# Kernel tuning notes

Hardware: AMD Instinct MI355X
Metric: run time of the kernel (lower is better)

Reference implementation:

```python
import jax, jax.numpy as jnp
import numpy as np

N, E, F, D = 50000, 800000, 128, 32
CUTOFF = 5.0


def swish(x):
    return x * jax.nn.sigmoid(x)


def setup_inputs() -> dict:
    key = jax.random.key(0)
    ks = jax.random.split(key, 15)
    sF = 1.0 / np.sqrt(F)
    inp = {
        "x": jax.random.normal(ks[0], (N, F), jnp.float32),
        # distances in [0, 6) so some edges lie beyond the 5.0 cutoff
        "rij": jax.random.uniform(ks[1], (E,), jnp.float32) * 6.0,
        "vij": jax.random.normal(ks[2], (E, 3), jnp.float32),
        "src": jax.random.randint(ks[3], (E,), 0, N),
        "dst": jax.random.randint(ks[4], (E,), 0, N),
        # transform: Dense(F,F,swish) -> Dense(F,D,swish)
        "W1": jax.random.normal(ks[5], (F, F), jnp.float32) * sF,
        "b1": jnp.zeros((F,), jnp.float32),
        "W2": jax.random.normal(ks[6], (F, D), jnp.float32) * sF,
        "b2": jnp.zeros((D,), jnp.float32),
        # transform2 (cross_product branch)
        "W1b": jax.random.normal(ks[7], (F, F), jnp.float32) * sF,
        "b1b": jnp.zeros((F,), jnp.float32),
        "W2b": jax.random.normal(ks[8], (F, D), jnp.float32) * sF,
        "b2b": jnp.zeros((D,), jnp.float32),
        # mix: Dense(3, 1), no activation
        "w_mix": jax.random.normal(ks[9], (3,), jnp.float32) * (1.0 / np.sqrt(3.0)),
        "b_mix": jnp.zeros((1,), jnp.float32),
    }
    return inp


def reference(x, rij, vij, src, dst, W1, b1, W2, b2, W1b, b1b, W2b, b2b, w_mix, b_mix):
    # node transforms: q, q2 in [N, D]
    q = swish(swish(x @ W1 + b1) @ W2 + b2)
    q2 = swish(swish(x @ W1b + b1b) @ W2b + b2b)

    # cosine cutoff on per-edge distance [E]
    c = 0.5 * (jnp.cos(jnp.pi * rij / CUTOFF) + 1.0)
    c = c * (rij < CUTOFF).astype(c.dtype)

    # e_mul_u: edge vij [E,1,3] * source-node q [E,D,1] -> [E,D,3], then cutoff scale
    mu_ij = vij[:, None, :] * q[src][:, :, None] * c[:, None, None]
    mu = jax.ops.segment_sum(mu_ij, dst, num_segments=N)  # [N,D,3]

    mu_ij2 = vij[:, None, :] * q2[src][:, :, None] * c[:, None, None]
    mu2 = jax.ops.segment_sum(mu_ij2, dst, num_segments=N)  # [N,D,3]

    mu3 = jnp.cross(mu, mu2, axis=-1)  # [N,D,3]
    stacked = jnp.stack([mu, mu2, mu3], axis=-1)  # [N,D,3,3]
    out = stacked @ w_mix + b_mix[0]  # mix Dense(3,1), squeezed -> [N,D,3]
    return out
```

## Files before the change

kernel.cpp:

```cpp
#include <hip/hip_runtime.h>
#include <hip/hip_bf16.h>

#define N_NODES 50000
#define E_EDGES 800000
#define F_DIM 128
#define D_DIM 32
#define CUTOFF 5.0f
#define PI_F 3.14159265358979f
#define SCAN_BLOCKS ((N_NODES + 255) / 256)

#define MLP_ROWBLOCKS 782
#define MLP_BLOCKS (MLP_ROWBLOCKS * 2)
#define HIST_BLOCKS ((E_EDGES + 511) / 512)
#define XPAD 132

__device__ __forceinline__ float swishf(float x) { return x / (1.0f + expf(-x)); }

__global__ __launch_bounds__(512, 4)
void mlp_hist(const float* __restrict__ x,
              const float* __restrict__ W1a, const float* __restrict__ b1a,
              const float* __restrict__ W2a, const float* __restrict__ b2a,
              const float* __restrict__ W1b, const float* __restrict__ b1b,
              const float* __restrict__ W2b, const float* __restrict__ b2b,
              float* __restrict__ qq,
              const float* __restrict__ rij, const int* __restrict__ dst,
              int* __restrict__ deg) {
  if (blockIdx.x >= MLP_BLOCKS) {
    const int e = (blockIdx.x - MLP_BLOCKS) * 512 + threadIdx.x;
    if (e < E_EDGES && rij[e] < CUTOFF) atomicAdd(&deg[dst[e]], 1);
    return;
  }

  __shared__ float sX[64 * XPAD];

  const int bid = blockIdx.x;
  const int br  = (bid >= MLP_ROWBLOCKS) ? 1 : 0;
  const int rb  = (bid - br * MLP_ROWBLOCKS) * 64;

  const float* __restrict__ W1 = br ? W1b : W1a;
  const float* __restrict__ b1 = br ? b1b : b1a;
  const float* __restrict__ W2 = br ? W2b : W2a;
  const float* __restrict__ b2 = br ? b2b : b2a;

  const int t = threadIdx.x;
  const int l = t & 63;
  const int w = t >> 6;

  {
    const int row = t >> 3;
    const int kq  = t & 7;
    const int rowG = min(rb + row, N_NODES - 1);
    const float* xp = x + (size_t)rowG * F_DIM;
#pragma unroll
    for (int p = 0; p < 4; ++p) {
      const int k0 = kq * 4 + p * 32;
      *(float4*)&sX[row * XPAD + k0] = *(const float4*)&xp[k0];
    }
  }
  __syncthreads();

  const int cb = l & 31;
  const int g  = (w << 1) + (l >> 5);
  const int r0 = g * 4;

  float acc[4][4];
#pragma unroll
  for (int j = 0; j < 4; ++j) {
    const float bj = b1[cb + 32 * j];
#pragma unroll
    for (int r = 0; r < 4; ++r) acc[r][j] = bj;
  }
  {
    const float* xrow = sX + r0 * XPAD;
#pragma unroll 2
    for (int k4 = 0; k4 < 32; ++k4) {
      float4 xv[4];
#pragma unroll
      for (int r = 0; r < 4; ++r)
        xv[r] = *(const float4*)&xrow[r * XPAD + k4 * 4];
#pragma unroll
      for (int kk = 0; kk < 4; ++kk) {
        const int k = k4 * 4 + kk;
        float wv[4];
#pragma unroll
        for (int j = 0; j < 4; ++j)
          wv[j] = W1[(size_t)k * F_DIM + cb + 32 * j];
#pragma unroll
        for (int r = 0; r < 4; ++r) {
          const float xs = (kk == 0) ? xv[r].x : (kk == 1) ? xv[r].y
                         : (kk == 2) ? xv[r].z : xv[r].w;
#pragma unroll
          for (int j = 0; j < 4; ++j)
            acc[r][j] = fmaf(xs, wv[j], acc[r][j]);
        }
      }
    }
  }

  __syncthreads();
#pragma unroll
  for (int r = 0; r < 4; ++r)
#pragma unroll
    for (int j = 0; j < 4; ++j)
      sX[(r0 + r) * XPAD + cb + 32 * j] = swishf(acc[r][j]);
  __syncthreads();

  float acc2[4];
  {
    const float b2c = b2[cb];
#pragma unroll
    for (int r = 0; r < 4; ++r) acc2[r] = b2c;
  }
  {
    const float* hrow = sX + r0 * XPAD;
#pragma unroll 2
    for (int k4 = 0; k4 < 32; ++k4) {
      float4 hv[4];
#pragma unroll
      for (int r = 0; r < 4; ++r)
        hv[r] = *(const float4*)&hrow[r * XPAD + k4 * 4];
#pragma unroll
      for (int kk = 0; kk < 4; ++kk) {
        const float wv = W2[(size_t)(k4 * 4 + kk) * D_DIM + cb];
#pragma unroll
        for (int r = 0; r < 4; ++r) {
          const float hs = (kk == 0) ? hv[r].x : (kk == 1) ? hv[r].y
                         : (kk == 2) ? hv[r].z : hv[r].w;
          acc2[r] = fmaf(hs, wv, acc2[r]);
        }
      }
    }
  }
#pragma unroll
  for (int r = 0; r < 4; ++r) {
    const int row = rb + r0 + r;
    if (row < N_NODES) qq[(size_t)row * 64 + 2 * cb + br] = swishf(acc2[r]);
  }
}

__global__ __launch_bounds__(256)
void scan_blocksum(const int* __restrict__ deg, int* __restrict__ part) {
  __shared__ int red[256];
  const int t = threadIdx.x;
  const int i = blockIdx.x * 256 + t;
  red[t] = (i < N_NODES) ? deg[i] : 0;
  __syncthreads();
#pragma unroll
  for (int off = 128; off > 0; off >>= 1) {
    if (t < off) red[t] += red[t + off];
    __syncthreads();
  }
  if (t == 0) part[blockIdx.x] = red[0];
}

__global__ __launch_bounds__(256)
void scan_partials(int* __restrict__ part, int* __restrict__ row_start) {
  __shared__ int s[256];
  const int t = threadIdx.x;
  const int v = (t < SCAN_BLOCKS) ? part[t] : 0;
  s[t] = v;
  __syncthreads();
  for (int off = 1; off < 256; off <<= 1) {
    const int u = (t >= off) ? s[t - off] : 0;
    __syncthreads();
    s[t] += u;
    __syncthreads();
  }
  if (t < SCAN_BLOCKS) part[t] = s[t] - v;
  if (t == 255) row_start[N_NODES] = s[255];
}

__global__ __launch_bounds__(256)
void scan_write(const int* __restrict__ deg, const int* __restrict__ part,
                int* __restrict__ row_start, int* __restrict__ cursor) {
  __shared__ int s[256];
  const int t = threadIdx.x;
  const int i = blockIdx.x * 256 + t;
  const int v = (i < N_NODES) ? deg[i] : 0;
  s[t] = v;
  __syncthreads();
  for (int off = 1; off < 256; off <<= 1) {
    const int u = (t >= off) ? s[t - off] : 0;
    __syncthreads();
    s[t] += u;
    __syncthreads();
  }
  const int excl = s[t] - v + part[blockIdx.x];
  if (i < N_NODES) { row_start[i] = excl; cursor[i] = excl; }
}

__global__ __launch_bounds__(256)
void edge_reorder(const float* __restrict__ rij, const float* __restrict__ vij,
                  const int* __restrict__ src, const int* __restrict__ dst,
                  int* __restrict__ cursor, float4* __restrict__ recs) {
  const int e = blockIdx.x * 256 + threadIdx.x;
  if (e >= E_EDGES) return;
  const float r = rij[e];
  if (r >= CUTOFF) return;
  const float c = 0.5f * (cosf(r * (PI_F / CUTOFF)) + 1.0f);
  const int pos = atomicAdd(&cursor[dst[e]], 1);
  recs[pos] = make_float4(c * vij[3 * e + 0], c * vij[3 * e + 1],
                          c * vij[3 * e + 2], __int_as_float(src[e]));
}

__global__ __launch_bounds__(256)
void gather_out(const int* __restrict__ row_start, const float4* __restrict__ recs,
                const float2* __restrict__ qq,
                const float* __restrict__ w_mix, const float* __restrict__ b_mix,
                float* __restrict__ out) {
  const int tid = blockIdx.x * 256 + threadIdx.x;
  const int n = tid >> 5;
  const int d = tid & 31;
  if (n >= N_NODES) return;

  const int s0 = row_start[n];
  const int s1 = row_start[n + 1];

  float ax = 0.f, ay = 0.f, az = 0.f, bx = 0.f, by = 0.f, bz = 0.f;
  for (int i = s0; i < s1; i += 4) {
    const int i1 = min(i + 1, s1 - 1);
    const int i2 = min(i + 2, s1 - 1);
    const int i3 = min(i + 3, s1 - 1);
    float4 rc0 = recs[i];
    float4 rc1 = recs[i1];
    float4 rc2 = recs[i2];
    float4 rc3 = recs[i3];
    float2 p0 = qq[__float_as_int(rc0.w) * 32 + d];
    float2 p1 = qq[__float_as_int(rc1.w) * 32 + d];
    float2 p2 = qq[__float_as_int(rc2.w) * 32 + d];
    float2 p3 = qq[__float_as_int(rc3.w) * 32 + d];
    const float m1 = (i + 1 < s1) ? 1.f : 0.f;
    const float m2 = (i + 2 < s1) ? 1.f : 0.f;
    const float m3 = (i + 3 < s1) ? 1.f : 0.f;
    p1.x *= m1; p1.y *= m1;
    p2.x *= m2; p2.y *= m2;
    p3.x *= m3; p3.y *= m3;

    ax += rc0.x * p0.x + rc1.x * p1.x + rc2.x * p2.x + rc3.x * p3.x;
    ay += rc0.y * p0.x + rc1.y * p1.x + rc2.y * p2.x + rc3.y * p3.x;
    az += rc0.z * p0.x + rc1.z * p1.x + rc2.z * p2.x + rc3.z * p3.x;
    bx += rc0.x * p0.y + rc1.x * p1.y + rc2.x * p2.y + rc3.x * p3.y;
    by += rc0.y * p0.y + rc1.y * p1.y + rc2.y * p2.y + rc3.y * p3.y;
    bz += rc0.z * p0.y + rc1.z * p1.y + rc2.z * p2.y + rc3.z * p3.y;
  }

  const float cx = ay * bz - az * by;
  const float cy = az * bx - ax * bz;
  const float cz = ax * by - ay * bx;

  const float w0 = w_mix[0], w1 = w_mix[1], w2 = w_mix[2];
  const float bm = b_mix[0];

  const size_t base = (size_t)tid * 3;
  out[base + 0] = ax * w0 + bx * w1 + cx * w2 + bm;
  out[base + 1] = ay * w0 + by * w1 + cy * w2 + bm;
  out[base + 2] = az * w0 + bz * w1 + cz * w2 + bm;
}

extern "C" void kernel_launch(void* const* d_in, const int* in_sizes, int n_in,
                              void* d_out, int out_size, void* d_ws, size_t ws_size,
                              hipStream_t stream) {
  const float* x     = (const float*)d_in[0];
  const float* rij   = (const float*)d_in[1];
  const float* vij   = (const float*)d_in[2];
  const int*   src   = (const int*)  d_in[3];
  const int*   dst   = (const int*)  d_in[4];
  const float* W1    = (const float*)d_in[5];
  const float* b1    = (const float*)d_in[6];
  const float* W2    = (const float*)d_in[7];
  const float* b2    = (const float*)d_in[8];
  const float* W1b   = (const float*)d_in[9];
  const float* b1b   = (const float*)d_in[10];
  const float* W2b   = (const float*)d_in[11];
  const float* b2b   = (const float*)d_in[12];
  const float* w_mix = (const float*)d_in[13];
  const float* b_mix = (const float*)d_in[14];
  float* out = (float*)d_out;

  float4* recs   = (float4*)d_ws;
  float* qq      = (float*)(recs + E_EDGES);
  int* deg       = (int*)(qq + (size_t)N_NODES * 64);
  int* cursor    = deg + N_NODES;
  int* row_start = cursor + N_NODES;
  int* part      = row_start + N_NODES + 1;

  hipMemsetAsync(deg, 0, sizeof(int) * N_NODES, stream);

  mlp_hist<<<MLP_BLOCKS + HIST_BLOCKS, 512, 0, stream>>>(
      x, W1, b1, W2, b2, W1b, b1b, W2b, b2b, qq, rij, dst, deg);

  scan_blocksum<<<SCAN_BLOCKS, 256, 0, stream>>>(deg, part);
  scan_partials<<<1, 256, 0, stream>>>(part, row_start);
  scan_write<<<SCAN_BLOCKS, 256, 0, stream>>>(deg, part, row_start, cursor);

  const int eb = (E_EDGES + 255) / 256;
  edge_reorder<<<eb, 256, 0, stream>>>(rij, vij, src, dst, cursor, recs);

  gather_out<<<(N_NODES * D_DIM) / 256, 256, 0, stream>>>(
      row_start, recs, (const float2*)qq, w_mix, b_mix, out);
}
```

Measured before the change: 280.0 us.

## Compute both MLP branches per block with larger per-thread register tiles

```diff
diff --git a/kernel.cpp b/kernel.cpp
--- a/kernel.cpp
+++ b/kernel.cpp
@@ -9,14 +9,13 @@
 #define PI_F 3.14159265358979f
 #define SCAN_BLOCKS ((N_NODES + 255) / 256)
 
-#define MLP_ROWBLOCKS 782
-#define MLP_BLOCKS (MLP_ROWBLOCKS * 2)
-#define HIST_BLOCKS ((E_EDGES + 511) / 512)
+#define MLP_BLOCKS ((N_NODES + 63) / 64)
+#define HIST_BLOCKS ((E_EDGES + 255) / 256)
 #define XPAD 132
 
 __device__ __forceinline__ float swishf(float x) { return x / (1.0f + expf(-x)); }
 
-__global__ __launch_bounds__(512, 4)
+__global__ __launch_bounds__(256, 4)
 void mlp_hist(const float* __restrict__ x,
               const float* __restrict__ W1a, const float* __restrict__ b1a,
               const float* __restrict__ W2a, const float* __restrict__ b2a,
@@ -26,115 +25,145 @@
               const float* __restrict__ rij, const int* __restrict__ dst,
               int* __restrict__ deg) {
   if (blockIdx.x >= MLP_BLOCKS) {
-    const int e = (blockIdx.x - MLP_BLOCKS) * 512 + threadIdx.x;
+    const int e = (blockIdx.x - MLP_BLOCKS) * 256 + threadIdx.x;
     if (e < E_EDGES && rij[e] < CUTOFF) atomicAdd(&deg[dst[e]], 1);
     return;
   }
 
   __shared__ float sX[64 * XPAD];
 
-  const int bid = blockIdx.x;
-  const int br  = (bid >= MLP_ROWBLOCKS) ? 1 : 0;
-  const int rb  = (bid - br * MLP_ROWBLOCKS) * 64;
-
-  const float* __restrict__ W1 = br ? W1b : W1a;
-  const float* __restrict__ b1 = br ? b1b : b1a;
-  const float* __restrict__ W2 = br ? W2b : W2a;
-  const float* __restrict__ b2 = br ? b2b : b2a;
-
-  const int t = threadIdx.x;
-  const int l = t & 63;
-  const int w = t >> 6;
-
-  {
-    const int row = t >> 3;
-    const int kq  = t & 7;
+  const int rb = blockIdx.x * 64;
+  const int t  = threadIdx.x;
+  const int c16 = t & 15;
+  const int r0  = (t >> 4) * 4;
+
+  float qo[2][4][2];
+
+  auto stage_x = [&]() {
+    const int row = t >> 2;
+    const int kq  = t & 3;
     const int rowG = min(rb + row, N_NODES - 1);
     const float* xp = x + (size_t)rowG * F_DIM;
 #pragma unroll
-    for (int p = 0; p < 4; ++p) {
-      const int k0 = kq * 4 + p * 32;
+    for (int p = 0; p < 8; ++p) {
+      const int k0 = kq * 4 + p * 16;
       *(float4*)&sX[row * XPAD + k0] = *(const float4*)&xp[k0];
     }
-  }
-  __syncthreads();
-
-  const int cb = l & 31;
-  const int g  = (w << 1) + (l >> 5);
-  const int r0 = g * 4;
-
-  float acc[4][4];
-#pragma unroll
-  for (int j = 0; j < 4; ++j) {
-    const float bj = b1[cb + 32 * j];
-#pragma unroll
-    for (int r = 0; r < 4; ++r) acc[r][j] = bj;
-  }
-  {
-    const float* xrow = sX + r0 * XPAD;
+  };
+
+#pragma unroll
+  for (int br = 0; br < 2; ++br) {
+    const float* __restrict__ W1 = br ? W1b : W1a;
+    const float* __restrict__ b1 = br ? b1b : b1a;
+    const float* __restrict__ W2 = br ? W2b : W2a;
+    const float* __restrict__ b2 = br ? b2b : b2a;
+
+    if (br) __syncthreads();
+    stage_x();
+    __syncthreads();
+
+    float acc[4][8];
+    {
+      const float4 bv0 = *(const float4*)&b1[8 * c16];
+      const float4 bv1 = *(const float4*)&b1[8 * c16 + 4];
+#pragma unroll
+      for (int r = 0; r < 4; ++r) {
+        acc[r][0] = bv0.x; acc[r][1] = bv0.y; acc[r][2] = bv0.z; acc[r][3] = bv0.w;
+        acc[r][4] = bv1.x; acc[r][5] = bv1.y; acc[r][6] = bv1.z; acc[r][7] = bv1.w;
+      }
+    }
+    {
+      const float* xrow  = sX + r0 * XPAD;
+      const float* wbase = W1 + 8 * c16;
 #pragma unroll 2
-    for (int k4 = 0; k4 < 32; ++k4) {
-      float4 xv[4];
-#pragma unroll
-      for (int r = 0; r < 4; ++r)
-        xv[r] = *(const float4*)&xrow[r * XPAD + k4 * 4];
-#pragma unroll
-      for (int kk = 0; kk < 4; ++kk) {
-        const int k = k4 * 4 + kk;
-        float wv[4];
-#pragma unroll
-        for (int j = 0; j < 4; ++j)
-          wv[j] = W1[(size_t)k * F_DIM + cb + 32 * j];
-#pragma unroll
-        for (int r = 0; r < 4; ++r) {
-          const float xs = (kk == 0) ? xv[r].x : (kk == 1) ? xv[r].y
-                         : (kk == 2) ? xv[r].z : xv[r].w;
-#pragma unroll
-          for (int j = 0; j < 4; ++j)
-            acc[r][j] = fmaf(xs, wv[j], acc[r][j]);
+      for (int k4 = 0; k4 < 32; ++k4) {
+        float4 w0[4], w1[4];
+#pragma unroll
+        for (int kk = 0; kk < 4; ++kk) {
+          const float* wp = wbase + (size_t)(k4 * 4 + kk) * F_DIM;
+          w0[kk] = *(const float4*)wp;
+          w1[kk] = *(const float4*)(wp + 4);
+        }
+        float4 xv[4];
+#pragma unroll
+        for (int r = 0; r < 4; ++r)
+          xv[r] = *(const float4*)&xrow[r * XPAD + k4 * 4];
+#pragma unroll
+        for (int kk = 0; kk < 4; ++kk) {
+#pragma unroll
+          for (int r = 0; r < 4; ++r) {
+            const float xs = (kk == 0) ? xv[r].x : (kk == 1) ? xv[r].y
+                           : (kk == 2) ? xv[r].z : xv[r].w;
+            acc[r][0] = fmaf(xs, w0[kk].x, acc[r][0]);
+            acc[r][1] = fmaf(xs, w0[kk].y, acc[r][1]);
+            acc[r][2] = fmaf(xs, w0[kk].z, acc[r][2]);
+            acc[r][3] = fmaf(xs, w0[kk].w, acc[r][3]);
+            acc[r][4] = fmaf(xs, w1[kk].x, acc[r][4]);
+            acc[r][5] = fmaf(xs, w1[kk].y, acc[r][5]);
+            acc[r][6] = fmaf(xs, w1[kk].z, acc[r][6]);
+            acc[r][7] = fmaf(xs, w1[kk].w, acc[r][7]);
+          }
         }
       }
     }
-  }
-
-  __syncthreads();
-#pragma unroll
-  for (int r = 0; r < 4; ++r)
-#pragma unroll
-    for (int j = 0; j < 4; ++j)
-      sX[(r0 + r) * XPAD + cb + 32 * j] = swishf(acc[r][j]);
-  __syncthreads();
-
-  float acc2[4];
-  {
-    const float b2c = b2[cb];
-#pragma unroll
-    for (int r = 0; r < 4; ++r) acc2[r] = b2c;
-  }
-  {
-    const float* hrow = sX + r0 * XPAD;
+
+    __syncthreads();
+#pragma unroll
+    for (int r = 0; r < 4; ++r) {
+      *(float4*)&sX[(r0 + r) * XPAD + 8 * c16] =
+          make_float4(swishf(acc[r][0]), swishf(acc[r][1]),
+                      swishf(acc[r][2]), swishf(acc[r][3]));
+      *(float4*)&sX[(r0 + r) * XPAD + 8 * c16 + 4] =
+          make_float4(swishf(acc[r][4]), swishf(acc[r][5]),
+                      swishf(acc[r][6]), swishf(acc[r][7]));
+    }
+    __syncthreads();
+
+    float a2[4][2];
+    {
+      const float2 b2v = *(const float2*)&b2[2 * c16];
+#pragma unroll
+      for (int r = 0; r < 4; ++r) { a2[r][0] = b2v.x; a2[r][1] = b2v.y; }
+    }
+    {
+      const float* hrow = sX + r0 * XPAD;
 #pragma unroll 2
-    for (int k4 = 0; k4 < 32; ++k4) {
-      float4 hv[4];
-#pragma unroll
-      for (int r = 0; r < 4; ++r)
-        hv[r] = *(const float4*)&hrow[r * XPAD + k4 * 4];
-#pragma unroll
-      for (int kk = 0; kk < 4; ++kk) {
-        const float wv = W2[(size_t)(k4 * 4 + kk) * D_DIM + cb];
-#pragma unroll
-        for (int r = 0; r < 4; ++r) {
-          const float hs = (kk == 0) ? hv[r].x : (kk == 1) ? hv[r].y
-                         : (kk == 2) ? hv[r].z : hv[r].w;
-          acc2[r] = fmaf(hs, wv, acc2[r]);
+      for (int k4 = 0; k4 < 32; ++k4) {
+        float2 wv[4];
+#pragma unroll
+        for (int kk = 0; kk < 4; ++kk)
+          wv[kk] = *(const float2*)&W2[(size_t)(k4 * 4 + kk) * D_DIM + 2 * c16];
+        float4 hv[4];
+#pragma unroll
+        for (int r = 0; r < 4; ++r)
+          hv[r] = *(const float4*)&hrow[r * XPAD + k4 * 4];
+#pragma unroll
+        for (int kk = 0; kk < 4; ++kk) {
+#pragma unroll
+          for (int r = 0; r < 4; ++r) {
+            const float hs = (kk == 0) ? hv[r].x : (kk == 1) ? hv[r].y
+                           : (kk == 2) ? hv[r].z : hv[r].w;
+            a2[r][0] = fmaf(hs, wv[kk].x, a2[r][0]);
+            a2[r][1] = fmaf(hs, wv[kk].y, a2[r][1]);
+          }
         }
       }
     }
-  }
+#pragma unroll
+    for (int r = 0; r < 4; ++r) {
+      qo[br][r][0] = a2[r][0];
+      qo[br][r][1] = a2[r][1];
+    }
+  }
+
 #pragma unroll
   for (int r = 0; r < 4; ++r) {
     const int row = rb + r0 + r;
-    if (row < N_NODES) qq[(size_t)row * 64 + 2 * cb + br] = swishf(acc2[r]);
+    if (row < N_NODES) {
+      *(float4*)&qq[(size_t)row * 64 + 4 * c16] =
+          make_float4(swishf(qo[0][r][0]), swishf(qo[1][r][0]),
+                      swishf(qo[0][r][1]), swishf(qo[1][r][1]));
+    }
   }
 }
 
@@ -286,7 +315,7 @@
 
   hipMemsetAsync(deg, 0, sizeof(int) * N_NODES, stream);
 
-  mlp_hist<<<MLP_BLOCKS + HIST_BLOCKS, 512, 0, stream>>>(
+  mlp_hist<<<MLP_BLOCKS + HIST_BLOCKS, 256, 0, stream>>>(
       x, W1, b1, W2, b2, W1b, b1b, W2b, b2b, qq, rij, dst, deg);
 
   scan_blocksum<<<SCAN_BLOCKS, 256, 0, stream>>>(deg, part);
```

After: 286.9 us. +2.5%, slower.

## Compute both MLP branches per block to share the staged x tile

Applied to the files above, without the earlier changes.

```diff
diff --git a/kernel.cpp b/kernel.cpp
--- a/kernel.cpp
+++ b/kernel.cpp
@@ -9,14 +9,13 @@
 #define PI_F 3.14159265358979f
 #define SCAN_BLOCKS ((N_NODES + 255) / 256)
 
-#define MLP_ROWBLOCKS 782
-#define MLP_BLOCKS (MLP_ROWBLOCKS * 2)
-#define HIST_BLOCKS ((E_EDGES + 511) / 512)
+#define MLP_BLOCKS ((N_NODES + 31) / 32)
+#define HIST_BLOCKS ((E_EDGES + 255) / 256)
 #define XPAD 132
 
 __device__ __forceinline__ float swishf(float x) { return x / (1.0f + expf(-x)); }
 
-__global__ __launch_bounds__(512, 4)
+__global__ __launch_bounds__(256, 4)
 void mlp_hist(const float* __restrict__ x,
               const float* __restrict__ W1a, const float* __restrict__ b1a,
               const float* __restrict__ W2a, const float* __restrict__ b2a,
@@ -26,25 +25,17 @@
               const float* __restrict__ rij, const int* __restrict__ dst,
               int* __restrict__ deg) {
   if (blockIdx.x >= MLP_BLOCKS) {
-    const int e = (blockIdx.x - MLP_BLOCKS) * 512 + threadIdx.x;
+    const int e = (blockIdx.x - MLP_BLOCKS) * 256 + threadIdx.x;
     if (e < E_EDGES && rij[e] < CUTOFF) atomicAdd(&deg[dst[e]], 1);
     return;
   }
 
   __shared__ float sX[64 * XPAD];
 
-  const int bid = blockIdx.x;
-  const int br  = (bid >= MLP_ROWBLOCKS) ? 1 : 0;
-  const int rb  = (bid - br * MLP_ROWBLOCKS) * 64;
-
-  const float* __restrict__ W1 = br ? W1b : W1a;
-  const float* __restrict__ b1 = br ? b1b : b1a;
-  const float* __restrict__ W2 = br ? W2b : W2a;
-  const float* __restrict__ b2 = br ? b2b : b2a;
-
-  const int t = threadIdx.x;
-  const int l = t & 63;
-  const int w = t >> 6;
+  const int rb = blockIdx.x * 32;
+  const int t  = threadIdx.x;
+  const int c  = t & 31;
+  const int r0 = (t >> 5) * 4;
 
   {
     const int row = t >> 3;
@@ -59,39 +50,47 @@
   }
   __syncthreads();
 
-  const int cb = l & 31;
-  const int g  = (w << 1) + (l >> 5);
-  const int r0 = g * 4;
-
-  float acc[4][4];
-#pragma unroll
-  for (int j = 0; j < 4; ++j) {
-    const float bj = b1[cb + 32 * j];
-#pragma unroll
-    for (int r = 0; r < 4; ++r) acc[r][j] = bj;
+  float accA[4][4], accB[4][4];
+  {
+    const float4 ba = *(const float4*)&b1a[4 * c];
+    const float4 bb = *(const float4*)&b1b[4 * c];
+#pragma unroll
+    for (int r = 0; r < 4; ++r) {
+      accA[r][0] = ba.x; accA[r][1] = ba.y; accA[r][2] = ba.z; accA[r][3] = ba.w;
+      accB[r][0] = bb.x; accB[r][1] = bb.y; accB[r][2] = bb.z; accB[r][3] = bb.w;
+    }
   }
   {
     const float* xrow = sX + r0 * XPAD;
+    const float* wa_base = W1a + 4 * c;
+    const float* wb_base = W1b + 4 * c;
 #pragma unroll 2
     for (int k4 = 0; k4 < 32; ++k4) {
+      float4 wa[4], wb[4];
+#pragma unroll
+      for (int kk = 0; kk < 4; ++kk) {
+        const size_t off = (size_t)(k4 * 4 + kk) * F_DIM;
+        wa[kk] = *(const float4*)(wa_base + off);
+        wb[kk] = *(const float4*)(wb_base + off);
+      }
       float4 xv[4];
 #pragma unroll
       for (int r = 0; r < 4; ++r)
         xv[r] = *(const float4*)&xrow[r * XPAD + k4 * 4];
 #pragma unroll
       for (int kk = 0; kk < 4; ++kk) {
-        const int k = k4 * 4 + kk;
-        float wv[4];
-#pragma unroll
-        for (int j = 0; j < 4; ++j)
-          wv[j] = W1[(size_t)k * F_DIM + cb + 32 * j];
 #pragma unroll
         for (int r = 0; r < 4; ++r) {
           const float xs = (kk == 0) ? xv[r].x : (kk == 1) ? xv[r].y
                          : (kk == 2) ? xv[r].z : xv[r].w;
-#pragma unroll
-          for (int j = 0; j < 4; ++j)
-            acc[r][j] = fmaf(xs, wv[j], acc[r][j]);
+          accA[r][0] = fmaf(xs, wa[kk].x, accA[r][0]);
+          accA[r][1] = fmaf(xs, wa[kk].y, accA[r][1]);
+          accA[r][2] = fmaf(xs, wa[kk].z, accA[r][2]);
+          accA[r][3] = fmaf(xs, wa[kk].w, accA[r][3]);
+          accB[r][0] = fmaf(xs, wb[kk].x, accB[r][0]);
+          accB[r][1] = fmaf(xs, wb[kk].y, accB[r][1]);
+          accB[r][2] = fmaf(xs, wb[kk].z, accB[r][2]);
+          accB[r][3] = fmaf(xs, wb[kk].w, accB[r][3]);
         }
       }
     }
@@ -99,42 +98,62 @@
 
   __syncthreads();
 #pragma unroll
-  for (int r = 0; r < 4; ++r)
-#pragma unroll
-    for (int j = 0; j < 4; ++j)
-      sX[(r0 + r) * XPAD + cb + 32 * j] = swishf(acc[r][j]);
-  __syncthreads();
-
-  float acc2[4];
-  {
-    const float b2c = b2[cb];
-#pragma unroll
-    for (int r = 0; r < 4; ++r) acc2[r] = b2c;
-  }
-  {
-    const float* hrow = sX + r0 * XPAD;
+  for (int r = 0; r < 4; ++r) {
+    *(float4*)&sX[(r0 + r) * XPAD + 4 * c] =
+        make_float4(swishf(accA[r][0]), swishf(accA[r][1]),
+                    swishf(accA[r][2]), swishf(accA[r][3]));
+    *(float4*)&sX[(32 + r0 + r) * XPAD + 4 * c] =
+        make_float4(swishf(accB[r][0]), swishf(accB[r][1]),
+                    swishf(accB[r][2]), swishf(accB[r][3]));
+  }
+  __syncthreads();
+
+  float a2A[4], a2B[4];
+  {
+    const float bA = b2a[c];
+    const float bB = b2b[c];
+#pragma unroll
+    for (int r = 0; r < 4; ++r) { a2A[r] = bA; a2B[r] = bB; }
+  }
+  {
+    const float* hrowA = sX + r0 * XPAD;
+    const float* hrowB = sX + (32 + r0) * XPAD;
 #pragma unroll 2
     for (int k4 = 0; k4 < 32; ++k4) {
-      float4 hv[4];
-#pragma unroll
-      for (int r = 0; r < 4; ++r)
-        hv[r] = *(const float4*)&hrow[r * XPAD + k4 * 4];
+      float wA[4], wB[4];
 #pragma unroll
       for (int kk = 0; kk < 4; ++kk) {
-        const float wv = W2[(size_t)(k4 * 4 + kk) * D_DIM + cb];
+        wA[kk] = W2a[(size_t)(k4 * 4 + kk) * D_DIM + c];
+        wB[kk] = W2b[(size_t)(k4 * 4 + kk) * D_DIM + c];
+      }
+      float4 hA[4], hB[4];
+#pragma unroll
+      for (int r = 0; r < 4; ++r) {
+        hA[r] = *(const float4*)&hrowA[r * XPAD + k4 * 4];
+        hB[r] = *(const float4*)&hrowB[r * XPAD + k4 * 4];
+      }
+#pragma unroll
+      for (int kk = 0; kk < 4; ++kk) {
 #pragma unroll
         for (int r = 0; r < 4; ++r) {
-          const float hs = (kk == 0) ? hv[r].x : (kk == 1) ? hv[r].y
-                         : (kk == 2) ? hv[r].z : hv[r].w;
-          acc2[r] = fmaf(hs, wv, acc2[r]);
+          const float hsA = (kk == 0) ? hA[r].x : (kk == 1) ? hA[r].y
+                          : (kk == 2) ? hA[r].z : hA[r].w;
+          const float hsB = (kk == 0) ? hB[r].x : (kk == 1) ? hB[r].y
+                          : (kk == 2) ? hB[r].z : hB[r].w;
+          a2A[r] = fmaf(hsA, wA[kk], a2A[r]);
+          a2B[r] = fmaf(hsB, wB[kk], a2B[r]);
         }
       }
     }
   }
+
 #pragma unroll
   for (int r = 0; r < 4; ++r) {
     const int row = rb + r0 + r;
-    if (row < N_NODES) qq[(size_t)row * 64 + 2 * cb + br] = swishf(acc2[r]);
+    if (row < N_NODES) {
+      *(float2*)&qq[(size_t)row * 64 + 2 * c] =
+          make_float2(swishf(a2A[r]), swishf(a2B[r]));
+    }
   }
 }
 
@@ -286,7 +305,7 @@
 
   hipMemsetAsync(deg, 0, sizeof(int) * N_NODES, stream);
 
-  mlp_hist<<<MLP_BLOCKS + HIST_BLOCKS, 512, 0, stream>>>(
+  mlp_hist<<<MLP_BLOCKS + HIST_BLOCKS, 256, 0, stream>>>(
       x, W1, b1, W2, b2, W1b, b1b, W2b, b2b, qq, rij, dst, deg);
 
   scan_blocksum<<<SCAN_BLOCKS, 256, 0, stream>>>(deg, part);
```

Result: no change. 279.8 us (-0.1%).

## Fuse both MLP branches per block and merge scan passes into one kernel

Applied to the files above, without the earlier changes.

```diff
diff --git a/kernel.cpp b/kernel.cpp
--- a/kernel.cpp
+++ b/kernel.cpp
@@ -9,14 +9,14 @@
 #define PI_F 3.14159265358979f
 #define SCAN_BLOCKS ((N_NODES + 255) / 256)
 
-#define MLP_ROWBLOCKS 782
-#define MLP_BLOCKS (MLP_ROWBLOCKS * 2)
-#define HIST_BLOCKS ((E_EDGES + 511) / 512)
+#define MLP_BLOCKS ((N_NODES + 31) / 32)
+#define HIST_BLOCKS ((E_EDGES + 255) / 256)
 #define XPAD 132
+#define SQ_STRIDE 66
 
 __device__ __forceinline__ float swishf(float x) { return x / (1.0f + expf(-x)); }
 
-__global__ __launch_bounds__(512, 4)
+__global__ __launch_bounds__(256, 4)
 void mlp_hist(const float* __restrict__ x,
               const float* __restrict__ W1a, const float* __restrict__ b1a,
               const float* __restrict__ W2a, const float* __restrict__ b2a,
@@ -26,25 +26,17 @@
               const float* __restrict__ rij, const int* __restrict__ dst,
               int* __restrict__ deg) {
   if (blockIdx.x >= MLP_BLOCKS) {
-    const int e = (blockIdx.x - MLP_BLOCKS) * 512 + threadIdx.x;
+    const int e = (blockIdx.x - MLP_BLOCKS) * 256 + threadIdx.x;
     if (e < E_EDGES && rij[e] < CUTOFF) atomicAdd(&deg[dst[e]], 1);
     return;
   }
 
   __shared__ float sX[64 * XPAD];
 
-  const int bid = blockIdx.x;
-  const int br  = (bid >= MLP_ROWBLOCKS) ? 1 : 0;
-  const int rb  = (bid - br * MLP_ROWBLOCKS) * 64;
-
-  const float* __restrict__ W1 = br ? W1b : W1a;
-  const float* __restrict__ b1 = br ? b1b : b1a;
-  const float* __restrict__ W2 = br ? W2b : W2a;
-  const float* __restrict__ b2 = br ? b2b : b2a;
-
-  const int t = threadIdx.x;
-  const int l = t & 63;
-  const int w = t >> 6;
+  const int rb = blockIdx.x * 32;
+  const int t  = threadIdx.x;
+  const int w  = t >> 6;
+  const int l  = t & 63;
 
   {
     const int row = t >> 3;
@@ -59,82 +51,99 @@
   }
   __syncthreads();
 
-  const int cb = l & 31;
-  const int g  = (w << 1) + (l >> 5);
-  const int r0 = g * 4;
-
-  float acc[4][4];
-#pragma unroll
-  for (int j = 0; j < 4; ++j) {
-    const float bj = b1[cb + 32 * j];
-#pragma unroll
-    for (int r = 0; r < 4; ++r) acc[r][j] = bj;
-  }
-  {
-    const float* xrow = sX + r0 * XPAD;
+  const int h1    = l >> 5;
+  const int cl    = l & 31;
+  const int col   = w * 32 + cl;
+  const int rbase = h1 * 16;
+
+  float accA[16], accB[16];
+  {
+    const float bA = b1a[col];
+    const float bB = b1b[col];
+#pragma unroll
+    for (int r = 0; r < 16; ++r) { accA[r] = bA; accB[r] = bB; }
+  }
+  {
+    const float* xrow = sX + rbase * XPAD;
 #pragma unroll 2
     for (int k4 = 0; k4 < 32; ++k4) {
-      float4 xv[4];
-#pragma unroll
-      for (int r = 0; r < 4; ++r)
-        xv[r] = *(const float4*)&xrow[r * XPAD + k4 * 4];
+      float wa[4], wb[4];
 #pragma unroll
       for (int kk = 0; kk < 4; ++kk) {
-        const int k = k4 * 4 + kk;
-        float wv[4];
-#pragma unroll
-        for (int j = 0; j < 4; ++j)
-          wv[j] = W1[(size_t)k * F_DIM + cb + 32 * j];
-#pragma unroll
-        for (int r = 0; r < 4; ++r) {
-          const float xs = (kk == 0) ? xv[r].x : (kk == 1) ? xv[r].y
-                         : (kk == 2) ? xv[r].z : xv[r].w;
-#pragma unroll
-          for (int j = 0; j < 4; ++j)
-            acc[r][j] = fmaf(xs, wv[j], acc[r][j]);
-        }
+        const size_t off = (size_t)(k4 * 4 + kk) * F_DIM + col;
+        wa[kk] = W1a[off];
+        wb[kk] = W1b[off];
+      }
+#pragma unroll
+      for (int r = 0; r < 16; ++r) {
+        const float4 xv = *(const float4*)&xrow[r * XPAD + k4 * 4];
+        accA[r] = fmaf(xv.x, wa[0], accA[r]);
+        accA[r] = fmaf(xv.y, wa[1], accA[r]);
+        accA[r] = fmaf(xv.z, wa[2], accA[r]);
+        accA[r] = fmaf(xv.w, wa[3], accA[r]);
+        accB[r] = fmaf(xv.x, wb[0], accB[r]);
+        accB[r] = fmaf(xv.y, wb[1], accB[r]);
+        accB[r] = fmaf(xv.z, wb[2], accB[r]);
+        accB[r] = fmaf(xv.w, wb[3], accB[r]);
       }
     }
   }
 
   __syncthreads();
 #pragma unroll
-  for (int r = 0; r < 4; ++r)
-#pragma unroll
-    for (int j = 0; j < 4; ++j)
-      sX[(r0 + r) * XPAD + cb + 32 * j] = swishf(acc[r][j]);
-  __syncthreads();
-
-  float acc2[4];
-  {
-    const float b2c = b2[cb];
-#pragma unroll
-    for (int r = 0; r < 4; ++r) acc2[r] = b2c;
-  }
-  {
-    const float* hrow = sX + r0 * XPAD;
+  for (int r = 0; r < 16; ++r) {
+    sX[(rbase + r) * XPAD + col]      = swishf(accA[r]);
+    sX[(32 + rbase + r) * XPAD + col] = swishf(accB[r]);
+  }
+  __syncthreads();
+
+  const int s   = w * 16 + (l & 15);
+  const int rq  = l >> 4;
+  const int br2 = s >> 5;
+  const int c2  = s & 31;
+
+  const float* __restrict__ W2 = br2 ? W2b : W2a;
+  const float* hbase = sX + (br2 ? 32 : 0) * XPAD + (rq * 8) * XPAD;
+
+  float acc2[8];
+  {
+    const float b2v = (br2 ? b2b : b2a)[c2];
+#pragma unroll
+    for (int r = 0; r < 8; ++r) acc2[r] = b2v;
+  }
 #pragma unroll 2
-    for (int k4 = 0; k4 < 32; ++k4) {
-      float4 hv[4];
-#pragma unroll
-      for (int r = 0; r < 4; ++r)
-        hv[r] = *(const float4*)&hrow[r * XPAD + k4 * 4];
-#pragma unroll
-      for (int kk = 0; kk < 4; ++kk) {
-        const float wv = W2[(size_t)(k4 * 4 + kk) * D_DIM + cb];
-#pragma unroll
-        for (int r = 0; r < 4; ++r) {
-          const float hs = (kk == 0) ? hv[r].x : (kk == 1) ? hv[r].y
-                         : (kk == 2) ? hv[r].z : hv[r].w;
-          acc2[r] = fmaf(hs, wv, acc2[r]);
-        }
-      }
+  for (int k4 = 0; k4 < 32; ++k4) {
+    float w2v[4];
+#pragma unroll
+    for (int kk = 0; kk < 4; ++kk)
+      w2v[kk] = W2[(size_t)(k4 * 4 + kk) * D_DIM + c2];
+#pragma unroll
+    for (int r = 0; r < 8; ++r) {
+      const float4 hv = *(const float4*)&hbase[r * XPAD + k4 * 4];
+      acc2[r] = fmaf(hv.x, w2v[0], acc2[r]);
+      acc2[r] = fmaf(hv.y, w2v[1], acc2[r]);
+      acc2[r] = fmaf(hv.z, w2v[2], acc2[r]);
+      acc2[r] = fmaf(hv.w, w2v[3], acc2[r]);
     }
   }
-#pragma unroll
-  for (int r = 0; r < 4; ++r) {
-    const int row = rb + r0 + r;
-    if (row < N_NODES) qq[(size_t)row * 64 + 2 * cb + br] = swishf(acc2[r]);
+
+  __syncthreads();
+#pragma unroll
+  for (int r = 0; r < 8; ++r)
+    sX[(rq * 8 + r) * SQ_STRIDE + 2 * c2 + br2] = swishf(acc2[r]);
+  __syncthreads();
+
+  {
+    const int row = t >> 3;
+    const int m   = t & 7;
+    if (rb + row < N_NODES) {
+      const float* sq = &sX[row * SQ_STRIDE + m * 8];
+      float4 v0 = *(const float4*)&sq[0];
+      float4 v1 = *(const float4*)&sq[4];
+      float* qp = &qq[(size_t)(rb + row) * 64 + m * 8];
+      *(float4*)&qp[0] = v0;
+      *(float4*)&qp[4] = v1;
+    }
   }
 }
 
@@ -154,27 +163,22 @@
 }
 
 __global__ __launch_bounds__(256)
-void scan_partials(int* __restrict__ part, int* __restrict__ row_start) {
+void scan_finish(const int* __restrict__ deg, const int* __restrict__ part,
+                 int* __restrict__ row_start, int* __restrict__ cursor) {
+  __shared__ int sp[256];
   __shared__ int s[256];
   const int t = threadIdx.x;
-  const int v = (t < SCAN_BLOCKS) ? part[t] : 0;
-  s[t] = v;
+  sp[t] = (t < SCAN_BLOCKS) ? part[t] : 0;
   __syncthreads();
   for (int off = 1; off < 256; off <<= 1) {
-    const int u = (t >= off) ? s[t - off] : 0;
-    __syncthreads();
-    s[t] += u;
-    __syncthreads();
-  }
-  if (t < SCAN_BLOCKS) part[t] = s[t] - v;
-  if (t == 255) row_start[N_NODES] = s[255];
-}
-
-__global__ __launch_bounds__(256)
-void scan_write(const int* __restrict__ deg, const int* __restrict__ part,
-                int* __restrict__ row_start, int* __restrict__ cursor) {
-  __shared__ int s[256];
-  const int t = threadIdx.x;
+    const int u = (t >= off) ? sp[t - off] : 0;
+    __syncthreads();
+    sp[t] += u;
+    __syncthreads();
+  }
+  const int bofs = (blockIdx.x > 0) ? sp[blockIdx.x - 1] : 0;
+  if (blockIdx.x == 0 && t == 0) row_start[N_NODES] = sp[SCAN_BLOCKS - 1];
+
   const int i = blockIdx.x * 256 + t;
   const int v = (i < N_NODES) ? deg[i] : 0;
   s[t] = v;
@@ -185,7 +189,7 @@
     s[t] += u;
     __syncthreads();
   }
-  const int excl = s[t] - v + part[blockIdx.x];
+  const int excl = s[t] - v + bofs;
   if (i < N_NODES) { row_start[i] = excl; cursor[i] = excl; }
 }
 
@@ -286,12 +290,11 @@
 
   hipMemsetAsync(deg, 0, sizeof(int) * N_NODES, stream);
 
-  mlp_hist<<<MLP_BLOCKS + HIST_BLOCKS, 512, 0, stream>>>(
+  mlp_hist<<<MLP_BLOCKS + HIST_BLOCKS, 256, 0, stream>>>(
       x, W1, b1, W2, b2, W1b, b1b, W2b, b2b, qq, rij, dst, deg);
 
   scan_blocksum<<<SCAN_BLOCKS, 256, 0, stream>>>(deg, part);
-  scan_partials<<<1, 256, 0, stream>>>(part, row_start);
-  scan_write<<<SCAN_BLOCKS, 256, 0, stream>>>(deg, part, row_start, cursor);
+  scan_finish<<<SCAN_BLOCKS, 256, 0, stream>>>(deg, part, row_start, cursor);
 
   const int eb = (E_EDGES + 255) / 256;
   edge_reorder<<<eb, 256, 0, stream>>>(rij, vij, src, dst, cursor, recs);
```

After: 285.4 us. No clear change (+1.9%).
